# Optimization experiments

Hardware: AMD Instinct MI355X
Metric: run time of the kernel (lower is better)

Reference implementation:

```python
import jax, jax.numpy as jnp
import numpy as np

N = 200000      # active voxels
K = 27          # kernel volume (3x3x3)
M = 50000       # rulebook pairs per kernel offset
CIN = 64
COUT = 64


def setup_inputs() -> dict:
    key = jax.random.key(0)
    k1, k2, k3, k4 = jax.random.split(key, 4)
    feats = jax.random.normal(k1, (N, CIN), dtype=jnp.float32)
    std = 1.0 / np.sqrt(CIN * K)
    kernel = jax.random.uniform(k2, (K, CIN, COUT), dtype=jnp.float32,
                                minval=-std, maxval=std)
    in_map = jax.random.randint(k3, (K, M), 0, N, dtype=jnp.int32)
    out_map = jax.random.randint(k4, (K, M), 0, N, dtype=jnp.int32)
    return {"feats": feats, "kernel": kernel, "in_map": in_map, "out_map": out_map}


def reference(feats, kernel, in_map, out_map):
    # gather: [K, M, Cin]
    gathered = feats[in_map]
    # per-offset GEMM: [K, M, Cout]
    partial = jnp.einsum('kmi,kio->kmo', gathered, kernel)
    # scatter-add into output features [N, Cout]
    out = jnp.zeros((feats.shape[0], kernel.shape[-1]), dtype=feats.dtype)
    out = out.at[out_map].add(partial)
    return out
```

## Files before the change

kernel.cpp:

```cpp
#include <hip/hip_runtime.h>
#include <hip/hip_fp16.h>

#define CIN   64
#define COUT  64

typedef __attribute__((ext_vector_type(8))) short bf16x8;
typedef __attribute__((ext_vector_type(4))) float f32x4;

__device__ inline unsigned short f2bf(float f) {
    unsigned u = __float_as_uint(f);
    return (unsigned short)((u + 0x7FFFu + ((u >> 16) & 1u)) >> 16);
}

__device__ inline unsigned pack_h2(float lo, float hi) {
    __half l = __float2half(lo), h = __float2half(hi);
    return (unsigned)__half_as_ushort(l) | ((unsigned)__half_as_ushort(h) << 16);
}

__global__ __launch_bounds__(256)
void hist_kernel(const int* __restrict__ out_map, int total, int* __restrict__ cnt) {
    int g = blockIdx.x * 256 + threadIdx.x;
    if (g >= total) return;
    atomicAdd(&cnt[out_map[g]], 1);
}

__global__ __launch_bounds__(256)
void scanA(const int* __restrict__ cnt, int* __restrict__ excl,
           int* __restrict__ blocksum, int N) {
    __shared__ int sm[256];
    const int b = blockIdx.x, t = threadIdx.x;
    const int base = b * 1024 + t * 4;
    int v0 = (base + 0 < N) ? cnt[base + 0] : 0;
    int v1 = (base + 1 < N) ? cnt[base + 1] : 0;
    int v2 = (base + 2 < N) ? cnt[base + 2] : 0;
    int v3 = (base + 3 < N) ? cnt[base + 3] : 0;
    const int s = v0 + v1 + v2 + v3;
    sm[t] = s; __syncthreads();
    for (int off = 1; off < 256; off <<= 1) {
        int x = (t >= off) ? sm[t - off] : 0;
        __syncthreads();
        sm[t] += x;
        __syncthreads();
    }
    const int e = sm[t] - s;
    if (t == 255) blocksum[b] = sm[t];
    if (base + 0 < N) excl[base + 0] = e;
    if (base + 1 < N) excl[base + 1] = e + v0;
    if (base + 2 < N) excl[base + 2] = e + v0 + v1;
    if (base + 3 < N) excl[base + 3] = e + v0 + v1 + v2;
}

__global__ __launch_bounds__(256)
void scanB(const int* __restrict__ blocksum, int* __restrict__ blockbase,
           int nb, int* __restrict__ total_out) {
    __shared__ int sm[256];
    const int t = threadIdx.x;
    const int s = (t < nb) ? blocksum[t] : 0;
    sm[t] = s; __syncthreads();
    for (int off = 1; off < 256; off <<= 1) {
        int x = (t >= off) ? sm[t - off] : 0;
        __syncthreads();
        sm[t] += x;
        __syncthreads();
    }
    if (t < nb) blockbase[t] = sm[t] - s;
    if (t == 255) *total_out = sm[255];
}

__global__ __launch_bounds__(256)
void scanC(int* __restrict__ offsets, int* __restrict__ ofs_work,
           const int* __restrict__ blockbase, int N) {
    int i = blockIdx.x * 256 + threadIdx.x;
    if (i >= N) return;
    const int v = offsets[i] + blockbase[i >> 10];
    offsets[i]  = v;
    ofs_work[i] = v;
}

__global__ __launch_bounds__(256)
void fill_kernel(const int* __restrict__ out_map, int total,
                 int* __restrict__ ofs_work, int* __restrict__ slot) {
    int g = blockIdx.x * 256 + threadIdx.x;
    if (g >= total) return;
    slot[g] = atomicAdd(&ofs_work[out_map[g]], 1);
}

__global__ __launch_bounds__(256)
void cvt_feats(const float4* __restrict__ in, unsigned short* __restrict__ outb,
               int n8) {
    int i = blockIdx.x * 256 + threadIdx.x;
    if (i >= n8) return;
    float4 f0 = in[2 * i], f1 = in[2 * i + 1];
    bf16x8 o;
    o[0] = (short)f2bf(f0.x); o[1] = (short)f2bf(f0.y);
    o[2] = (short)f2bf(f0.z); o[3] = (short)f2bf(f0.w);
    o[4] = (short)f2bf(f1.x); o[5] = (short)f2bf(f1.y);
    o[6] = (short)f2bf(f1.z); o[7] = (short)f2bf(f1.w);
    *(bf16x8*)(outb + 8 * (size_t)i) = o;
}

__global__ __launch_bounds__(256)
void spconv_phase1(const unsigned short* __restrict__ featsb,
                   const float*          __restrict__ weight,
                   const int*            __restrict__ in_map,
                   const int*            __restrict__ slot,
                   unsigned*             __restrict__ partial_dw,
                   int M) {
    const int k      = blockIdx.y;
    const int tid    = threadIdx.x;
    const int lane   = tid & 63;
    const int m      = lane & 15;
    const int quad   = lane >> 4;
    const int wave   = blockIdx.x * 4 + (tid >> 6);
    const int nwaves = gridDim.x * 4;
    const bool odd   = (m & 1);

    const float* __restrict__ wk = weight + (size_t)k * (CIN * COUT);
    bf16x8 bfrag[4][2];
#pragma unroll
    for (int t = 0; t < 4; ++t)
#pragma unroll
        for (int h = 0; h < 2; ++h) {
            const int n  = 16 * t + m;
            const int c0 = 32 * h + 8 * quad;
#pragma unroll
            for (int j = 0; j < 8; ++j)
                bfrag[t][h][j] = (short)f2bf(wk[(c0 + j) * COUT + n]);
        }

    const int base   = k * M;
    const int ntiles = M >> 4;

    for (int tile = wave; tile < ntiles; tile += nwaves) {
        const int p0     = tile << 4;
        const int in_row = in_map[base + p0 + m];
        const int slt    = slot[base + p0 + m];

        const unsigned short* fb = featsb + ((size_t)in_row << 6) + 8 * quad;
        const bf16x8 a0 = *(const bf16x8*)fb;
        const bf16x8 a1 = *(const bf16x8*)(fb + 32);

        f32x4 acc[4];
#pragma unroll
        for (int t = 0; t < 4; ++t) {
            acc[t] = {0.f, 0.f, 0.f, 0.f};
            acc[t] = __builtin_amdgcn_mfma_f32_16x16x32_bf16(a0, bfrag[t][0], acc[t], 0, 0, 0);
            acc[t] = __builtin_amdgcn_mfma_f32_16x16x32_bf16(a1, bfrag[t][1], acc[t], 0, 0, 0);
        }

        const int row0  = 4 * quad + (odd ? 2 : 0);
        const int s0    = __shfl(slt, row0);
        const int s1    = __shfl(slt, row0 + 1);
        const int coldw = m >> 1;
#pragma unroll
        for (int t = 0; t < 4; ++t) {
            const float send0 = odd ? acc[t][0] : acc[t][2];
            const float send1 = odd ? acc[t][1] : acc[t][3];
            const float recv0 = __shfl_xor(send0, 1);
            const float recv1 = __shfl_xor(send1, 1);

            const unsigned d0 = odd ? pack_h2(recv0, acc[t][2])
                                    : pack_h2(acc[t][0], recv0);
            const unsigned d1 = odd ? pack_h2(recv1, acc[t][3])
                                    : pack_h2(acc[t][1], recv1);

            partial_dw[(size_t)s0 * 32 + coldw + 8 * t] = d0;
            partial_dw[(size_t)s1 * 32 + coldw + 8 * t] = d1;
        }
    }
}

__global__ __launch_bounds__(256)
void spconv_phase2(const unsigned* __restrict__ partial_dw,
                   const int*      __restrict__ offsets,
                   float2*         __restrict__ out,
                   int nrows) {
    const int tid  = threadIdx.x;
    const int lane = tid & 63;
    const int half = lane >> 5;
    const int c2   = lane & 31;
    const int wave = blockIdx.x * 4 + (tid >> 6);
    const int nw   = gridDim.x * 4;

    for (int r = wave; r < nrows; r += nw) {
        const int start = offsets[r];
        const int c     = offsets[r + 1] - start;

        float ax = 0.f, ay = 0.f;
        for (int j0 = 0; j0 < c; j0 += 8) {
#pragma unroll
            for (int u = 0; u < 4; ++u) {
                const int j = j0 + 2 * u + half;
                if (j < c) {
                    const unsigned v = partial_dw[(size_t)(start + j) * 32 + c2];
                    ax += __half2float(__ushort_as_half((unsigned short)(v & 0xFFFF)));
                    ay += __half2float(__ushort_as_half((unsigned short)(v >> 16)));
                }
            }
        }

        ax += __shfl_xor(ax, 32);
        ay += __shfl_xor(ay, 32);
        if (half == 0)
            out[(size_t)r * 32 + c2] = make_float2(ax, ay);
    }
}

__global__ __launch_bounds__(256)
void spconv_atomic(const float* __restrict__ feats,
                   const float* __restrict__ weight,
                   const int*   __restrict__ in_map,
                   const int*   __restrict__ out_map,
                   float*       __restrict__ out,
                   int M) {
    const int k      = blockIdx.y;
    const int tid    = threadIdx.x;
    const int lane   = tid & 63;
    const int m      = lane & 15;
    const int quad   = lane >> 4;
    const int wave   = blockIdx.x * 4 + (tid >> 6);
    const int nwaves = gridDim.x * 4;

    const float* __restrict__ wk = weight + (size_t)k * (CIN * COUT);
    bf16x8 bfrag[4][2];
#pragma unroll
    for (int t = 0; t < 4; ++t)
#pragma unroll
        for (int h = 0; h < 2; ++h) {
            const int n  = 16 * t + m;
            const int c0 = 32 * h + 8 * quad;
#pragma unroll
            for (int j = 0; j < 8; ++j)
                bfrag[t][h][j] = (short)f2bf(wk[(c0 + j) * COUT + n]);
        }

    const int base   = k * M;
    const int ntiles = M >> 4;

    for (int tile = wave; tile < ntiles; tile += nwaves) {
        const int p0 = tile << 4;
        const int in_row  = in_map[base + p0 + m];
        const int out_row = out_map[base + p0 + m];

        const float* __restrict__ fr = feats + ((size_t)in_row << 6) + 8 * quad;
        const f32x4 f0 = *(const f32x4*)(fr + 0);
        const f32x4 f1 = *(const f32x4*)(fr + 4);
        const f32x4 f2 = *(const f32x4*)(fr + 32);
        const f32x4 f3 = *(const f32x4*)(fr + 36);

        bf16x8 a0, a1;
#pragma unroll
        for (int j = 0; j < 4; ++j) {
            a0[j]     = (short)f2bf(f0[j]);
            a0[j + 4] = (short)f2bf(f1[j]);
            a1[j]     = (short)f2bf(f2[j]);
            a1[j + 4] = (short)f2bf(f3[j]);
        }

        int orow[4];
#pragma unroll
        for (int r = 0; r < 4; ++r)
            orow[r] = __shfl(out_row, 4 * quad + r);

        f32x4 acc[4];
#pragma unroll
        for (int t = 0; t < 4; ++t) {
            acc[t] = {0.f, 0.f, 0.f, 0.f};
            acc[t] = __builtin_amdgcn_mfma_f32_16x16x32_bf16(a0, bfrag[t][0], acc[t], 0, 0, 0);
            acc[t] = __builtin_amdgcn_mfma_f32_16x16x32_bf16(a1, bfrag[t][1], acc[t], 0, 0, 0);
        }

#pragma unroll
        for (int t = 0; t < 4; ++t)
#pragma unroll
            for (int r = 0; r < 4; ++r)
                atomicAdd(out + (size_t)orow[r] * COUT + 16 * t + m, acc[t][r]);
    }
}

__global__ __launch_bounds__(256)
void zero_out_kernel(float4* __restrict__ out, int n4) {
    int i = blockIdx.x * 256 + threadIdx.x;
    if (i < n4) out[i] = make_float4(0.f, 0.f, 0.f, 0.f);
}

static inline size_t al256(size_t x) { return (x + 255) & ~(size_t)255; }

extern "C" void kernel_launch(void* const* d_in, const int* in_sizes, int n_in,
                              void* d_out, int out_size, void* d_ws, size_t ws_size,
                              hipStream_t stream) {
    const float* feats   = (const float*)d_in[0];
    const float* weight  = (const float*)d_in[1];
    const int*   in_map  = (const int*)d_in[2];
    const int*   out_map = (const int*)d_in[3];
    float*       out     = (float*)d_out;

    const int K     = in_sizes[1] / (CIN * COUT);
    const int M     = in_sizes[2] / K;
    const int N     = out_size / COUT;
    const int total = K * M;
    const int nb    = (N + 1023) >> 10;

    const size_t off_b  = al256((size_t)(N + 1) * 4);
    const size_t work_b = al256((size_t)N * 4);
    const size_t bs_b   = al256((size_t)nb * 4);
    const size_t bb_b   = al256((size_t)nb * 4);
    const size_t slot_b = al256((size_t)total * 4);
    const size_t fb_b   = al256((size_t)N * CIN * 2);
    const size_t part_b = (size_t)total * COUT * 2;
    const size_t need   = off_b + work_b + bs_b + bb_b + slot_b + fb_b + part_b;

    if ((M & 15) == 0 && nb <= 256 && ws_size >= need) {
        char* p = (char*)d_ws;
        int*            offsets   = (int*)p;            p += off_b;
        int*            ofs_work  = (int*)p;            p += work_b;
        int*            blocksum  = (int*)p;            p += bs_b;
        int*            blockbase = (int*)p;            p += bb_b;
        int*            slot      = (int*)p;            p += slot_b;
        unsigned short* featsb    = (unsigned short*)p; p += fb_b;
        unsigned*       partial   = (unsigned*)p;

        hipMemsetAsync(ofs_work, 0, (size_t)N * 4, stream);
        hist_kernel<<<(total + 255) / 256, 256, 0, stream>>>(out_map, total, ofs_work);
        scanA<<<nb, 256, 0, stream>>>(ofs_work, offsets, blocksum, N);
        scanB<<<1, 256, 0, stream>>>(blocksum, blockbase, nb, offsets + N);
        scanC<<<(N + 255) / 256, 256, 0, stream>>>(offsets, ofs_work, blockbase, N);
        fill_kernel<<<(total + 255) / 256, 256, 0, stream>>>(out_map, total, ofs_work, slot);

        const int n8 = N * CIN / 8;
        cvt_feats<<<(n8 + 255) / 256, 256, 0, stream>>>((const float4*)feats, featsb, n8);

        dim3 g1(80, K);
        spconv_phase1<<<g1, 256, 0, stream>>>(featsb, weight, in_map, slot, partial, M);

        spconv_phase2<<<4096, 256, 0, stream>>>(partial, offsets, (float2*)out, N);
        return;
    }

    int n4 = out_size / 4;
    zero_out_kernel<<<(n4 + 255) / 256, 256, 0, stream>>>((float4*)out, n4);
    dim3 grid(80, K);
    spconv_atomic<<<grid, 256, 0, stream>>>(feats, weight, in_map, out_map, out, M);
}
```

Before: 363.8 us.

## Fuse feature conversion with histogram and move slot assignment into GEMM kernel

Merges the bf16 feature conversion and the out_map histogram into one launch, drops the separate fill kernel and the slot buffer by having the GEMM kernel claim scatter slots with atomics inline, prefetches the next row's offsets in the reduction kernel, and doubles the phase-2 grid. This removes two launches and a full pass over the rulebook plus a slot array write and read. The cost is atomic latency inside the MFMA loop, issued by only one quad and shared via shuffle, which may serialize on hot rows.

```diff
diff --git a/kernel.cpp b/kernel.cpp
--- a/kernel.cpp
+++ b/kernel.cpp
@@ -18,10 +18,21 @@
 }
 
 __global__ __launch_bounds__(256)
-void hist_kernel(const int* __restrict__ out_map, int total, int* __restrict__ cnt) {
-    int g = blockIdx.x * 256 + threadIdx.x;
-    if (g >= total) return;
-    atomicAdd(&cnt[out_map[g]], 1);
+void cvt_hist(const float4* __restrict__ in, unsigned short* __restrict__ outb,
+              int n8, const int* __restrict__ out_map, int total,
+              int* __restrict__ cnt) {
+    int i = blockIdx.x * 256 + threadIdx.x;
+    if (i < n8) {
+        float4 f0 = in[2 * i], f1 = in[2 * i + 1];
+        bf16x8 o;
+        o[0] = (short)f2bf(f0.x); o[1] = (short)f2bf(f0.y);
+        o[2] = (short)f2bf(f0.z); o[3] = (short)f2bf(f0.w);
+        o[4] = (short)f2bf(f1.x); o[5] = (short)f2bf(f1.y);
+        o[6] = (short)f2bf(f1.z); o[7] = (short)f2bf(f1.w);
+        *(bf16x8*)(outb + 8 * (size_t)i) = o;
+    }
+    if (i < total)
+        atomicAdd(&cnt[out_map[i]], 1);
 }
 
 __global__ __launch_bounds__(256)
@@ -78,32 +89,11 @@
 }
 
 __global__ __launch_bounds__(256)
-void fill_kernel(const int* __restrict__ out_map, int total,
-                 int* __restrict__ ofs_work, int* __restrict__ slot) {
-    int g = blockIdx.x * 256 + threadIdx.x;
-    if (g >= total) return;
-    slot[g] = atomicAdd(&ofs_work[out_map[g]], 1);
-}
-
-__global__ __launch_bounds__(256)
-void cvt_feats(const float4* __restrict__ in, unsigned short* __restrict__ outb,
-               int n8) {
-    int i = blockIdx.x * 256 + threadIdx.x;
-    if (i >= n8) return;
-    float4 f0 = in[2 * i], f1 = in[2 * i + 1];
-    bf16x8 o;
-    o[0] = (short)f2bf(f0.x); o[1] = (short)f2bf(f0.y);
-    o[2] = (short)f2bf(f0.z); o[3] = (short)f2bf(f0.w);
-    o[4] = (short)f2bf(f1.x); o[5] = (short)f2bf(f1.y);
-    o[6] = (short)f2bf(f1.z); o[7] = (short)f2bf(f1.w);
-    *(bf16x8*)(outb + 8 * (size_t)i) = o;
-}
-
-__global__ __launch_bounds__(256)
 void spconv_phase1(const unsigned short* __restrict__ featsb,
                    const float*          __restrict__ weight,
                    const int*            __restrict__ in_map,
-                   const int*            __restrict__ slot,
+                   const int*            __restrict__ out_map,
+                   int*                  __restrict__ ofs_work,
                    unsigned*             __restrict__ partial_dw,
                    int M) {
     const int k      = blockIdx.y;
@@ -132,9 +122,13 @@
     const int ntiles = M >> 4;
 
     for (int tile = wave; tile < ntiles; tile += nwaves) {
-        const int p0     = tile << 4;
-        const int in_row = in_map[base + p0 + m];
-        const int slt    = slot[base + p0 + m];
+        const int p0      = tile << 4;
+        const int in_row  = in_map[base + p0 + m];
+        const int out_row = out_map[base + p0 + m];
+
+        int slt = 0;
+        if (quad == 0)
+            slt = atomicAdd(&ofs_work[out_row], 1);
 
         const unsigned short* fb = featsb + ((size_t)in_row << 6) + 8 * quad;
         const bf16x8 a0 = *(const bf16x8*)fb;
@@ -182,9 +176,18 @@
     const int wave = blockIdx.x * 4 + (tid >> 6);
     const int nw   = gridDim.x * 4;
 
+    if (wave >= nrows) return;
+    int cur_s = offsets[wave];
+    int cur_e = offsets[wave + 1];
+
     for (int r = wave; r < nrows; r += nw) {
-        const int start = offsets[r];
-        const int c     = offsets[r + 1] - start;
+        const int start = cur_s;
+        const int c     = cur_e - start;
+        const int rn    = r + nw;
+        if (rn < nrows) {
+            cur_s = offsets[rn];
+            cur_e = offsets[rn + 1];
+        }
 
         float ax = 0.f, ay = 0.f;
         for (int j0 = 0; j0 < c; j0 += 8) {
@@ -305,10 +308,9 @@
     const size_t work_b = al256((size_t)N * 4);
     const size_t bs_b   = al256((size_t)nb * 4);
     const size_t bb_b   = al256((size_t)nb * 4);
-    const size_t slot_b = al256((size_t)total * 4);
     const size_t fb_b   = al256((size_t)N * CIN * 2);
     const size_t part_b = (size_t)total * COUT * 2;
-    const size_t need   = off_b + work_b + bs_b + bb_b + slot_b + fb_b + part_b;
+    const size_t need   = off_b + work_b + bs_b + bb_b + fb_b + part_b;
 
     if ((M & 15) == 0 && nb <= 256 && ws_size >= need) {
         char* p = (char*)d_ws;
@@ -316,24 +318,24 @@
         int*            ofs_work  = (int*)p;            p += work_b;
         int*            blocksum  = (int*)p;            p += bs_b;
         int*            blockbase = (int*)p;            p += bb_b;
-        int*            slot      = (int*)p;            p += slot_b;
         unsigned short* featsb    = (unsigned short*)p; p += fb_b;
         unsigned*       partial   = (unsigned*)p;
 
+        const int n8 = N * CIN / 8;
+        const int fused_n = (n8 > total) ? n8 : total;
+
         hipMemsetAsync(ofs_work, 0, (size_t)N * 4, stream);
-        hist_kernel<<<(total + 255) / 256, 256, 0, stream>>>(out_map, total, ofs_work);
+        cvt_hist<<<(fused_n + 255) / 256, 256, 0, stream>>>(
+            (const float4*)feats, featsb, n8, out_map, total, ofs_work);
         scanA<<<nb, 256, 0, stream>>>(ofs_work, offsets, blocksum, N);
         scanB<<<1, 256, 0, stream>>>(blocksum, blockbase, nb, offsets + N);
         scanC<<<(N + 255) / 256, 256, 0, stream>>>(offsets, ofs_work, blockbase, N);
-        fill_kernel<<<(total + 255) / 256, 256, 0, stream>>>(out_map, total, ofs_work, slot);
-
-        const int n8 = N * CIN / 8;
-        cvt_feats<<<(n8 + 255) / 256, 256, 0, stream>>>((const float4*)feats, featsb, n8);
 
         dim3 g1(80, K);
-        spconv_phase1<<<g1, 256, 0, stream>>>(featsb, weight, in_map, slot, partial, M);
-
-        spconv_phase2<<<4096, 256, 0, stream>>>(partial, offsets, (float2*)out, N);
+        spconv_phase1<<<g1, 256, 0, stream>>>(featsb, weight, in_map, out_map,
+                                              ofs_work, partial, M);
+
+        spconv_phase2<<<8192, 256, 0, stream>>>(partial, offsets, (float2*)out, N);
         return;
     }
 
```

Result: faster. 331.8 us (-8.8%).
